# Kernel tuning notes

Hardware: AMD Instinct MI355X
Metric: run time of the kernel (lower is better)

Reference implementation:

```python
import jax, jax.numpy as jnp
import numpy as np

NUM_GROUPS = 8
EPS = 1e-5


def setup_inputs() -> dict:
    key = jax.random.key(0)
    ks = jax.random.split(key, 7)
    b, c, h, w = 4, 256, 64, 64
    x = jax.random.normal(ks[0], (b, c, h, w), dtype=jnp.float32)
    gamma = jnp.ones((c,), dtype=jnp.float32)
    beta = jnp.zeros((c,), dtype=jnp.float32)
    # 1x1 convs stored as [out_ch, in_ch] matrices
    w_qkv = jax.random.normal(ks[1], (3 * c, c), dtype=jnp.float32) * (1.0 / np.sqrt(c))
    b_qkv = jax.random.normal(ks[2], (3 * c,), dtype=jnp.float32) * 0.01
    # NOTE: original zero-inits proj; use small random weights so the op is non-trivial
    w_proj = jax.random.normal(ks[3], (c, c), dtype=jnp.float32) * (1.0 / np.sqrt(c))
    b_proj = jax.random.normal(ks[4], (c,), dtype=jnp.float32) * 0.01
    return {"x": x, "gamma": gamma, "beta": beta, "w_qkv": w_qkv,
            "b_qkv": b_qkv, "w_proj": w_proj, "b_proj": b_proj}


def _group_norm(x, gamma, beta):
    b, c, h, w = x.shape
    xg = x.reshape(b, NUM_GROUPS, c // NUM_GROUPS, h, w)
    mean = jnp.mean(xg, axis=(2, 3, 4), keepdims=True)
    var = jnp.var(xg, axis=(2, 3, 4), keepdims=True)
    xg = (xg - mean) * jax.lax.rsqrt(var + EPS)
    x = xg.reshape(b, c, h, w)
    return x * gamma[None, :, None, None] + beta[None, :, None, None]


def reference(x, gamma, beta, w_qkv, b_qkv, w_proj, b_proj):
    b, c, h, w = x.shape
    n = h * w
    residual = x
    xn = _group_norm(x, gamma, beta)
    # 1x1 conv qkv: [b, 3c, h, w]
    qkv = jnp.einsum('bchw,oc->bohw', xn, w_qkv) + b_qkv[None, :, None, None]
    q, k, v = jnp.split(qkv, 3, axis=1)
    q = q.reshape(b, c, n).transpose(0, 2, 1)   # [b, n, c]
    k = k.reshape(b, c, n)                       # [b, c, n]
    v = v.reshape(b, c, n).transpose(0, 2, 1)   # [b, n, c]
    scale = 1.0 / jnp.sqrt(jnp.asarray(c, dtype=x.dtype))
    attn = jnp.einsum('bic,bcj->bij', q, k) * scale    # [b, n, n]
    attn = jax.nn.softmax(attn, axis=-1)
    out = jnp.einsum('bij,bjc->bic', attn, v)          # [b, n, c]
    out = out.transpose(0, 2, 1).reshape(b, c, h, w)
    out = jnp.einsum('bchw,oc->bohw', out, w_proj) + b_proj[None, :, None, None]
    return out + residual
```

## Files before the change

### kernel.cpp

```cpp
#include <hip/hip_runtime.h>
#include <math.h>

#define BB   4
#define CC   256
#define NN   4096
#define GG   8
#define CPG  32
#define EPSV 1e-5f
#define SCALE 0.0625f
#define NSPLIT 4
#define PSTR 40

typedef __attribute__((ext_vector_type(8))) short bf16x8;
typedef __attribute__((ext_vector_type(4))) float f32x4;

struct alignas(8) us4 { unsigned short x, y, z, w; };

static __device__ __forceinline__ unsigned short f2bf(float f) {
    union { float f; unsigned int u; } a; a.f = f;
    unsigned int r = a.u + 0x7fffu + ((a.u >> 16) & 1u);
    return (unsigned short)(r >> 16);
}
static __device__ __forceinline__ void async16(const unsigned short* g, unsigned short* l) {
    __builtin_amdgcn_global_load_lds(
        (const __attribute__((address_space(1))) unsigned int*)g,
        (__attribute__((address_space(3))) unsigned int*)l,
        16, 0, 0);
}

__global__ __launch_bounds__(256) void prep_kernel(
    const float* __restrict__ x, const float* __restrict__ w_qkv,
    const float* __restrict__ w_proj, float* __restrict__ partials,
    unsigned short* __restrict__ wbf)
{
    const int tid = threadIdx.x;
    if (blockIdx.x >= 256) {
        int idx = ((blockIdx.x - 256)*256 + tid) * 4;
        float4 v;
        if (idx < 196608) v = *(const float4*)(w_qkv + idx);
        else              v = *(const float4*)(w_proj + (idx - 196608));
        us4 h = { f2bf(v.x), f2bf(v.y), f2bf(v.z), f2bf(v.w) };
        *(us4*)(wbf + idx) = h;
        return;
    }
    const int bg = blockIdx.x >> 3, slice = blockIdx.x & 7;
    const float4* base = (const float4*)(x + (size_t)bg*CPG*NN + slice*16384);
    float s = 0.f, sq = 0.f;
    for (int i = tid; i < 4096; i += 256) {
        float4 v = base[i];
        s  += v.x + v.y + v.z + v.w;
        sq += v.x*v.x + v.y*v.y + v.z*v.z + v.w*v.w;
    }
    __shared__ float ls[256], lq[256];
    ls[tid] = s; lq[tid] = sq;
    __syncthreads();
    for (int off = 128; off > 0; off >>= 1) {
        if (tid < off) { ls[tid] += ls[tid+off]; lq[tid] += lq[tid+off]; }
        __syncthreads();
    }
    if (tid == 0) { partials[blockIdx.x*2] = ls[0]; partials[blockIdx.x*2+1] = lq[0]; }
}

__global__ __launch_bounds__(256) void norm_t_kernel(
    const float* __restrict__ x, const float* __restrict__ gamma,
    const float* __restrict__ beta, const float* __restrict__ partials,
    unsigned short* __restrict__ xnT)
{
    const int n0 = blockIdx.x * 64;
    const int c0 = blockIdx.y * 64;
    const int b  = blockIdx.z;
    const int tid = threadIdx.x;
    __shared__ unsigned short T[64*68];
    __shared__ float ssc[64], ssh[64];
    if (tid < 64) {
        int c = c0 + tid;
        int bg = b*GG + (c >> 5);
        float s = 0.f, sq = 0.f;
        for (int i = 0; i < 8; i++) {
            s  += partials[(bg*8 + i)*2];
            sq += partials[(bg*8 + i)*2 + 1];
        }
        const float cnt = (float)(CPG*NN);
        float mean = s / cnt;
        float var  = sq / cnt - mean*mean;
        float rstd = rsqrtf(var + EPSV);
        float g = gamma[c], be = beta[c];
        ssc[tid] = rstd*g;
        ssh[tid] = be - mean*rstd*g;
    }
    __syncthreads();
    {
        int cl = tid >> 4, n4 = tid & 15;
        for (int i = 0; i < 4; i++) {
            int c = cl + i*16;
            float4 v = *(const float4*)(x + ((size_t)(b*CC + c0 + c))*NN + n0 + n4*4);
            float sc = ssc[c], sh = ssh[c];
            T[(n4*4+0)*68 + c] = f2bf(v.x*sc + sh);
            T[(n4*4+1)*68 + c] = f2bf(v.y*sc + sh);
            T[(n4*4+2)*68 + c] = f2bf(v.z*sc + sh);
            T[(n4*4+3)*68 + c] = f2bf(v.w*sc + sh);
        }
    }
    __syncthreads();
    {
        int nl = tid >> 3, cs = tid & 7;
        for (int i = 0; i < 2; i++) {
            int n = nl + i*32;
            *(bf16x8*)(xnT + ((size_t)(b*NN + n0 + n))*CC + c0 + cs*8) =
                *(const bf16x8*)&T[n*68 + cs*8];
        }
    }
}

__global__ __launch_bounds__(256) void qkv_mfma_kernel(
    const unsigned short* __restrict__ xnT, const unsigned short* __restrict__ wbf,
    const float* __restrict__ b_qkv,
    unsigned short* __restrict__ qsw, unsigned short* __restrict__ ksw,
    unsigned short* __restrict__ vsw)
{
    const int tid  = threadIdx.x;
    const int wave = tid >> 6, lane = tid & 63;
    const int lrow = lane & 15, quad = lane >> 4;
    const int R0   = blockIdx.x * 128;
    const int b    = blockIdx.x >> 5;
    const int nb0  = (blockIdx.x & 31) * 128;
    const int oBase = blockIdx.y * 64;
    const int which = oBase >> 8;
    const int o0l   = oBase & 255;
    const bool isV  = (which == 2);
    const int wn = wave >> 1, wo = wave & 1;

    const unsigned short* Abase;
    const unsigned short* Bbase;
    if (!isV) {
        Abase = wbf + ((size_t)(oBase + lrow))*CC + quad*8;
        Bbase = xnT + ((size_t)(R0 + wave*32 + lrow))*CC + quad*8;
    } else {
        Abase = xnT + ((size_t)(R0 + wn*64 + lrow))*CC + quad*8;
        Bbase = wbf + ((size_t)(oBase + wo*32 + lrow))*CC + quad*8;
    }

    f32x4 acc[4][2];
    for (int s = 0; s < 4; s++) for (int t = 0; t < 2; t++)
        acc[s][t] = (f32x4){0.f, 0.f, 0.f, 0.f};

    for (int c0 = 0; c0 < CC; c0 += 32) {
        bf16x8 af[4], bfr[2];
        for (int s = 0; s < 4; s++) af[s]  = *(const bf16x8*)(Abase + s*16*CC + c0);
        for (int t = 0; t < 2; t++) bfr[t] = *(const bf16x8*)(Bbase + t*16*CC + c0);
        for (int s = 0; s < 4; s++)
            for (int t = 0; t < 2; t++)
                acc[s][t] = __builtin_amdgcn_mfma_f32_16x16x32_bf16(af[s], bfr[t], acc[s][t], 0, 0, 0);
    }

    __shared__ unsigned short lds[8192];

    if (!isV) {
        const float sc = (which == 0) ? SCALE : 1.0f;
        for (int s = 0; s < 4; s++) {
            float bias[4];
            for (int r = 0; r < 4; r++) bias[r] = b_qkv[oBase + s*16 + quad*4 + r];
            for (int t = 0; t < 2; t++) {
                us4 h;
                h.x = f2bf((acc[s][t][0] + bias[0]) * sc);
                h.y = f2bf((acc[s][t][1] + bias[1]) * sc);
                h.z = f2bf((acc[s][t][2] + bias[2]) * sc);
                h.w = f2bf((acc[s][t][3] + bias[3]) * sc);
                int chunk = (wave*2 + t)*2 + (s>>1);
                int pos = (((s*2 + (quad>>1)) & 3)*16 + lrow)*8 + (quad&1)*4;
                *(us4*)&lds[chunk*512 + pos] = h;
            }
        }
    } else {
        for (int s = 0; s < 4; s++)
            for (int t = 0; t < 2; t++) {
                int oc = o0l + wo*32 + t*16 + lrow;
                float bias = b_qkv[512 + oc];
                us4 h;
                h.x = f2bf(acc[s][t][0] + bias);
                h.y = f2bf(acc[s][t][1] + bias);
                h.z = f2bf(acc[s][t][2] + bias);
                h.w = f2bf(acc[s][t][3] + bias);
                int chunk = (wn*2 + (s>>1))*4 + wo*2 + t;
                int pos = (((s&1)*2 + (quad>>1))*16 + lrow)*8 + (quad&1)*4;
                *(us4*)&lds[chunk*512 + pos] = h;
            }
    }
    __syncthreads();

    if (!isV) {
        unsigned short* dst = (which == 0) ? qsw : ksw;
        for (int it = 0; it < 4; it++) {
            int f = it*4 + (tid>>6);
            int ng_l = f >> 1, kk_l = f & 1;
            size_t off = ((size_t)(b*256 + (nb0>>4) + ng_l)*8 + (o0l>>5) + kk_l)*512 + lane*8;
            *(bf16x8*)(dst + off) = *(const bf16x8*)&lds[f*512 + lane*8];
        }
    } else {
        for (int it = 0; it < 4; it++) {
            int f = it*4 + (tid>>6);
            int jg_l = f >> 2, ns_l = f & 3;
            size_t off = ((size_t)(b*128 + (nb0>>5) + jg_l)*16 + (o0l>>4) + ns_l)*512 + lane*8;
            *(bf16x8*)(vsw + off) = *(const bf16x8*)&lds[f*512 + lane*8];
        }
    }
}

__global__ __launch_bounds__(256, 2) void attn_mfma_kernel(
    const unsigned short* __restrict__ qsw, const unsigned short* __restrict__ ksw,
    const unsigned short* __restrict__ vsw,
    unsigned short* __restrict__ opart, float* __restrict__ lpart)
{
    const int tid  = threadIdx.x;
    const int wave = tid >> 6, lane = tid & 63;
    const int lrow = lane & 15, quad = lane >> 4;
    const int bx    = blockIdx.x;
    const int split = bx & 3;
    const int ig    = (bx >> 2) & 31;
    const int b     = bx >> 7;
    const int i0w   = ig*128 + wave*32;
    const int koff  = split * (NN / NSPLIT);
    const int NT    = (NN / NSPLIT) / 32;

    __shared__ unsigned short ldsK[8192];
    __shared__ unsigned short ldsV[2][8192];
    __shared__ unsigned short ldsP[4][32*PSTR];

    bf16x8 qf[2][8];
    {
        const unsigned short* qb = qsw + ((size_t)b << 20) + (size_t)i0w*256 + lane*8;
        for (int g = 0; g < 2; g++)
            for (int kk = 0; kk < 8; kk++)
                qf[g][kk] = *(const bf16x8*)(qb + g*4096 + kk*512);
    }

    f32x4 o_acc[2][16];
    for (int g = 0; g < 2; g++)
        for (int ns = 0; ns < 16; ns++)
            o_acc[g][ns] = (f32x4){0.f, 0.f, 0.f, 0.f};
    float lsum[2] = {0.f, 0.f};

    const unsigned short* kp = ksw + ((size_t)b << 20) + (size_t)koff*256 + wave*2048 + lane*8;
    const unsigned short* vp = vsw + ((size_t)b << 20) + (size_t)koff*256 + wave*2048 + lane*8;

    for (int t = 0; t < 4; t++) {
        async16(kp + t*512, ldsK + wave*2048 + t*512);
        async16(vp + t*512, ldsV[0] + wave*2048 + t*512);
    }
    __syncthreads();

    for (int jt = 0; jt < NT; jt++) {
        const int cur = jt & 1, nxt = cur ^ 1;

        if (jt + 1 < NT)
            for (int t = 0; t < 4; t++)
                async16(vp + (size_t)(jt+1)*8192 + t*512, ldsV[nxt] + wave*2048 + t*512);

        f32x4 s[2][2];
        for (int jg = 0; jg < 2; jg++)
            for (int g = 0; g < 2; g++)
                s[jg][g] = (f32x4){0.f, 0.f, 0.f, 0.f};
        for (int jg = 0; jg < 2; jg++)
            for (int kk = 0; kk < 8; kk++) {
                bf16x8 kf = *(const bf16x8*)(ldsK + (jg*8 + kk)*512 + lane*8);
                s[jg][0] = __builtin_amdgcn_mfma_f32_16x16x32_bf16(kf, qf[0][kk], s[jg][0], 0, 0, 0);
                s[jg][1] = __builtin_amdgcn_mfma_f32_16x16x32_bf16(kf, qf[1][kk], s[jg][1], 0, 0, 0);
            }

        unsigned short* pw = ldsP[wave];
        for (int jg = 0; jg < 2; jg++)
            for (int g = 0; g < 2; g++) {
                float p0 = __expf(s[jg][g][0]);
                float p1 = __expf(s[jg][g][1]);
                float p2 = __expf(s[jg][g][2]);
                float p3 = __expf(s[jg][g][3]);
                lsum[g] += p0 + p1 + p2 + p3;
                us4 h = { f2bf(p0), f2bf(p1), f2bf(p2), f2bf(p3) };
                *(us4*)(pw + (g*16 + lrow)*PSTR + jg*16 + quad*4) = h;
            }

        __syncthreads();

        if (jt + 1 < NT)
            for (int t = 0; t < 4; t++)
                async16(kp + (size_t)(jt+1)*8192 + t*512, ldsK + wave*2048 + t*512);

        bf16x8 pa[2];
        for (int g = 0; g < 2; g++)
            pa[g] = *(const bf16x8*)(pw + (g*16 + lrow)*PSTR + quad*8);

        const unsigned short* lv = ldsV[cur];
        for (int ns = 0; ns < 16; ns++) {
            bf16x8 vf = *(const bf16x8*)(lv + ns*512 + lane*8);
            o_acc[0][ns] = __builtin_amdgcn_mfma_f32_16x16x32_bf16(pa[0], vf, o_acc[0][ns], 0, 0, 0);
            o_acc[1][ns] = __builtin_amdgcn_mfma_f32_16x16x32_bf16(pa[1], vf, o_acc[1][ns], 0, 0, 0);
        }
        __syncthreads();
    }

    for (int g = 0; g < 2; g++) {
        float v = lsum[g];
        v += __shfl_xor(v, 16);
        v += __shfl_xor(v, 32);
        lsum[g] = v;
    }

    unsigned short* reg = &ldsV[0][0] + wave*4096;
    const size_t planeb = ((size_t)(split*BB + b)) << 20;
    for (int g = 0; g < 2; g++) {
        for (int ns = 0; ns < 16; ns++) {
            int kk = ns >> 1;
            int posbase = ((ns & 1)*2 + (lrow >> 3))*128 + (lrow & 7) + quad*32;
            for (int r = 0; r < 4; r++)
                reg[kk*512 + posbase + r*8] = f2bf(o_acc[g][ns][r]);
        }
        unsigned short* dst = opart + planeb + ((size_t)((i0w >> 4) + g))*4096;
        for (int kk = 0; kk < 8; kk++)
            *(bf16x8*)(dst + kk*512 + lane*8) = *(const bf16x8*)(reg + kk*512 + lane*8);
    }
    if (quad == 0)
        for (int g = 0; g < 2; g++)
            lpart[(size_t)(split*BB + b)*NN + i0w + g*16 + lrow] = lsum[g];
}

__global__ __launch_bounds__(256, 2) void proj_mfma_kernel(
    const unsigned short* __restrict__ opart, const float* __restrict__ lpart,
    const unsigned short* __restrict__ w2bf, const float* __restrict__ b_proj,
    const float* __restrict__ x, float* __restrict__ out)
{
    const int tid  = threadIdx.x;
    const int wave = tid >> 6, lane = tid & 63;
    const int lrow = lane & 15, quad = lane >> 4;
    const int rt = blockIdx.x >> 1;
    const int oh = blockIdx.x & 1;
    const int b  = rt >> 6;
    const int n0 = (rt & 63) * 64;

    const int rg = (n0 >> 4) + wave;
    const unsigned short* Ab = opart + ((size_t)b << 20) + (size_t)rg*4096 + lane*8;
    const size_t pstride = (size_t)BB << 20;

    f32x4 acc[8];
    for (int t = 0; t < 8; t++) acc[t] = (f32x4){0.f, 0.f, 0.f, 0.f};

    for (int kk = 0; kk < 8; kk++) {
        bf16x8 bfr[8];
        for (int t = 0; t < 8; t++)
            bfr[t] = *(const bf16x8*)(w2bf +
                ((size_t)(oh*128 + t*16 + lrow))*CC + kk*32 + quad*8);
        for (int sp = 0; sp < NSPLIT; sp++) {
            bf16x8 af = *(const bf16x8*)(Ab + (size_t)sp*pstride + kk*512);
            for (int t = 0; t < 8; t++)
                acc[t] = __builtin_amdgcn_mfma_f32_16x16x32_bf16(af, bfr[t], acc[t], 0, 0, 0);
        }
    }

    float sinv[4];
    for (int r = 0; r < 4; r++) {
        int n = n0 + wave*16 + quad*4 + r;
        float l = 0.f;
        for (int sp = 0; sp < NSPLIT; sp++)
            l += lpart[(size_t)(sp*BB + b)*NN + n];
        sinv[r] = 1.0f / l;
    }

    for (int t = 0; t < 8; t++) {
        int o = oh*128 + t*16 + lrow;
        int n = n0 + wave*16 + quad*4;
        size_t idx = ((size_t)(b*CC + o))*NN + n;
        float bias = b_proj[o];
        float4 xv = *(const float4*)(x + idx);
        float4 ov;
        ov.x = acc[t][0]*sinv[0] + bias + xv.x;
        ov.y = acc[t][1]*sinv[1] + bias + xv.y;
        ov.z = acc[t][2]*sinv[2] + bias + xv.z;
        ov.w = acc[t][3]*sinv[3] + bias + xv.w;
        *(float4*)(out + idx) = ov;
    }
}

extern "C" void kernel_launch(void* const* d_in, const int* in_sizes, int n_in,
                              void* d_out, int out_size, void* d_ws, size_t ws_size,
                              hipStream_t stream) {
    const float* x      = (const float*)d_in[0];
    const float* gamma  = (const float*)d_in[1];
    const float* beta   = (const float*)d_in[2];
    const float* w_qkv  = (const float*)d_in[3];
    const float* b_qkv  = (const float*)d_in[4];
    const float* w_proj = (const float*)d_in[5];
    const float* b_proj = (const float*)d_in[6];
    float* out = (float*)d_out;

    const size_t plane = (size_t)BB * NN * CC;
    unsigned short* xnT = (unsigned short*)d_ws;
    unsigned short* qsw = xnT + plane;
    unsigned short* ksw = qsw + plane;
    unsigned short* vsw = ksw + plane;
    unsigned short* wbf = vsw + plane;
    unsigned short* opart = wbf + 262144;
    float* lpart    = (float*)(opart + (size_t)NSPLIT*plane);
    float* partials = lpart + (size_t)NSPLIT*BB*NN;

    prep_kernel<<<512, 256, 0, stream>>>(x, w_qkv, w_proj, partials, wbf);

    dim3 gnt(64, 4, BB);
    norm_t_kernel<<<gnt, 256, 0, stream>>>(x, gamma, beta, partials, xnT);

    dim3 gq(128, 12);
    qkv_mfma_kernel<<<gq, 256, 0, stream>>>(xnT, wbf, b_qkv, qsw, ksw, vsw);

    attn_mfma_kernel<<<BB*32*NSPLIT, 256, 0, stream>>>(qsw, ksw, vsw, opart, lpart);

    proj_mfma_kernel<<<512, 256, 0, stream>>>(opart, lpart, wbf + 196608, b_proj, x, out);
}
```

Measured before the change: 219.4 us.

## Load K/V fragments directly from global memory instead of LDS staging

The attention kernel stops staging K and V tiles in shared memory with async global-to-LDS copies and block-wide barriers. Each wave now reads its K and V MFMA fragments straight from global memory, relying on L2/L1 to serve the reuse across the four waves. This removes both __syncthreads per tile and shrinks LDS use, but the four waves now issue redundant global loads and there is no explicit prefetch, so load latency may be exposed.

```diff
diff --git a/kernel.cpp b/kernel.cpp
--- a/kernel.cpp
+++ b/kernel.cpp
@@ -222,9 +222,8 @@
     const int koff  = split * (NN / NSPLIT);
     const int NT    = (NN / NSPLIT) / 32;
 
-    __shared__ unsigned short ldsK[8192];
-    __shared__ unsigned short ldsV[2][8192];
     __shared__ unsigned short ldsP[4][32*PSTR];
+    __shared__ unsigned short ldsE[4][4096];
 
     bf16x8 qf[2][8];
     {
@@ -240,35 +239,31 @@
             o_acc[g][ns] = (f32x4){0.f, 0.f, 0.f, 0.f};
     float lsum[2] = {0.f, 0.f};
 
-    const unsigned short* kp = ksw + ((size_t)b << 20) + (size_t)koff*256 + wave*2048 + lane*8;
-    const unsigned short* vp = vsw + ((size_t)b << 20) + (size_t)koff*256 + wave*2048 + lane*8;
-
-    for (int t = 0; t < 4; t++) {
-        async16(kp + t*512, ldsK + wave*2048 + t*512);
-        async16(vp + t*512, ldsV[0] + wave*2048 + t*512);
-    }
-    __syncthreads();
+    const unsigned short* kb = ksw + ((size_t)b << 20) + (size_t)koff*256 + lane*8;
+    const unsigned short* vb = vsw + ((size_t)b << 20) + (size_t)koff*256 + lane*8;
+
+    unsigned short* pw = ldsP[wave];
 
     for (int jt = 0; jt < NT; jt++) {
-        const int cur = jt & 1, nxt = cur ^ 1;
-
-        if (jt + 1 < NT)
-            for (int t = 0; t < 4; t++)
-                async16(vp + (size_t)(jt+1)*8192 + t*512, ldsV[nxt] + wave*2048 + t*512);
+        const unsigned short* kt = kb + (size_t)jt*8192;
+        const unsigned short* vt = vb + (size_t)jt*8192;
 
         f32x4 s[2][2];
         for (int jg = 0; jg < 2; jg++)
             for (int g = 0; g < 2; g++)
                 s[jg][g] = (f32x4){0.f, 0.f, 0.f, 0.f};
+        #pragma unroll
         for (int jg = 0; jg < 2; jg++)
+            #pragma unroll
             for (int kk = 0; kk < 8; kk++) {
-                bf16x8 kf = *(const bf16x8*)(ldsK + (jg*8 + kk)*512 + lane*8);
+                bf16x8 kf = *(const bf16x8*)(kt + (jg*8 + kk)*512);
                 s[jg][0] = __builtin_amdgcn_mfma_f32_16x16x32_bf16(kf, qf[0][kk], s[jg][0], 0, 0, 0);
                 s[jg][1] = __builtin_amdgcn_mfma_f32_16x16x32_bf16(kf, qf[1][kk], s[jg][1], 0, 0, 0);
             }
 
-        unsigned short* pw = ldsP[wave];
+        #pragma unroll
         for (int jg = 0; jg < 2; jg++)
+            #pragma unroll
             for (int g = 0; g < 2; g++) {
                 float p0 = __expf(s[jg][g][0]);
                 float p1 = __expf(s[jg][g][1]);
@@ -279,23 +274,16 @@
                 *(us4*)(pw + (g*16 + lrow)*PSTR + jg*16 + quad*4) = h;
             }
 
-        __syncthreads();
-
-        if (jt + 1 < NT)
-            for (int t = 0; t < 4; t++)
-                async16(kp + (size_t)(jt+1)*8192 + t*512, ldsK + wave*2048 + t*512);
-
         bf16x8 pa[2];
         for (int g = 0; g < 2; g++)
             pa[g] = *(const bf16x8*)(pw + (g*16 + lrow)*PSTR + quad*8);
 
-        const unsigned short* lv = ldsV[cur];
+        #pragma unroll
         for (int ns = 0; ns < 16; ns++) {
-            bf16x8 vf = *(const bf16x8*)(lv + ns*512 + lane*8);
+            bf16x8 vf = *(const bf16x8*)(vt + ns*512);
             o_acc[0][ns] = __builtin_amdgcn_mfma_f32_16x16x32_bf16(pa[0], vf, o_acc[0][ns], 0, 0, 0);
             o_acc[1][ns] = __builtin_amdgcn_mfma_f32_16x16x32_bf16(pa[1], vf, o_acc[1][ns], 0, 0, 0);
         }
-        __syncthreads();
     }
 
     for (int g = 0; g < 2; g++) {
@@ -305,7 +293,7 @@
         lsum[g] = v;
     }
 
-    unsigned short* reg = &ldsV[0][0] + wave*4096;
+    unsigned short* reg = ldsE[wave];
     const size_t planeb = ((size_t)(split*BB + b)) << 20;
     for (int g = 0; g < 2; g++) {
         for (int ns = 0; ns < 16; ns++) {
```

New measurement: 315.3 us. +43.7%, slower.
